# Kernel tuning notes

Hardware: AMD Instinct MI355X
Metric: run time of the kernel (lower is better)

## Reference

```python
import jax, jax.numpy as jnp
import numpy as np

E = 131072
MS, MV = 64, 32            # node/edge/out irreps: 64x0e + 32x1o (dim 160)
DIM = MS + 3 * MV
SC = 64                    # edge scalar dim
BETA = 1.6791767           # normalize2mom(silu) constant used by e3nn FullyConnectedNet
SQ3 = np.float32(np.sqrt(3.0))


def _split(x, ms, mv):
    # e3nn layout: [mul_s scalars | mul_v vectors (mul-major, xyz-minor)]
    return x[:, :ms], x[:, ms:].reshape(x.shape[0], mv, 3)


def _tp(xs, xv, ys, yv, Wss, Wvv, Wsv, Wvs):
    # uvw fully-connected tensor product of (m1s x0e + m1v x1o) with (1x0e + 1x1o),
    # component irrep normalization, 1/sqrt(fan_in) path weights.
    m1s, m1v = xs.shape[1], xv.shape[1]
    s_a = jnp.einsum('eu,uw->ew', xs * ys, Wss) / np.sqrt(m1s)              # 0e x 0e -> 0e
    dot = jnp.einsum('eui,ei->eu', xv, yv) / SQ3                            # 1o x 1o -> 0e
    s_b = jnp.einsum('eu,uw->ew', dot, Wvv) / np.sqrt(m1v)
    v_a = jnp.einsum('eu,ei,uw->ewi', xs, yv, Wsv) / np.sqrt(m1s)           # 0e x 1o -> 1o
    v_b = jnp.einsum('eui,uw->ewi', xv * ys[:, :, None], Wvs) / np.sqrt(m1v)  # 1o x 0e -> 1o
    return jnp.concatenate([s_a, s_b], 1), jnp.concatenate([v_a, v_b], 1)


def _mlp(x, W1, W2, W3):
    # e3nn FullyConnectedNet with silu: variance-preserving layers
    h = BETA * jax.nn.silu(x @ W1 / np.sqrt(W1.shape[0]))
    h = BETA * jax.nn.silu(h @ W2 / np.sqrt(W2.shape[0]))
    return h @ W3 / np.sqrt(W3.shape[0])


def _scale_linear(ms_, mv_, w, Wls, Wlv):
    # LinearScaleWithWeights: per-channel (uvu) scale by generated weights, then o3.Linear
    nS = ms_.shape[1]
    s = ms_ * w[:, :nS]
    v = mv_ * w[:, nS:, None]
    s2 = s @ Wls / np.sqrt(Wls.shape[0])
    v2 = jnp.einsum('eui,uw->ewi', v, Wlv) / np.sqrt(Wlv.shape[0])
    return s2, v2


def _linear(s, v, Ws, Wv):
    return s @ Ws / np.sqrt(Ws.shape[0]), jnp.einsum('eui,uw->ewi', v, Wv) / np.sqrt(Wv.shape[0])


def setup_inputs() -> dict:
    key = jax.random.key(0)
    ks = jax.random.split(key, 32)
    r = lambda i, shp: jax.random.normal(ks[i], shp, dtype=jnp.float32)
    return {
        'node_feats_src': r(0, (E, DIM)),
        'node_feats_dst': r(1, (E, DIM)),
        'edge_feats':     r(2, (E, DIM)),
        'local_env_edge': r(3, (E, 4)),
        'edge_scalars':   r(4, (E, SC)),
        # node TP (combined 128x0e+64x1o x 1x0e+1x1o -> 128x0e+64x1o)
        'Wn_ss': r(5, (2 * MS, MS)), 'Wn_vv': r(6, (2 * MV, MS)),
        'Wn_sv': r(7, (2 * MS, MV)), 'Wn_vs': r(8, (2 * MV, MV)),
        # edge TP (64x0e+32x1o x 1x0e+1x1o -> 128x0e+64x1o)
        'We_ss': r(9, (MS, MS)), 'We_vv': r(10, (MV, MS)),
        'We_sv': r(11, (MS, MV)), 'We_vs': r(12, (MV, MV)),
        # scaler output linears (128x0e+64x1o -> 64x0e+32x1o)
        'Wns_s': r(13, (2 * MS, MS)), 'Wns_v': r(14, (2 * MV, MV)),
        'Wes_s': r(15, (2 * MS, MS)), 'Wes_v': r(16, (2 * MV, MV)),
        # final output linears (irreps_out -> irreps_out)
        'Wno_s': r(17, (MS, MS)), 'Wno_v': r(18, (MV, MV)),
        'Weo_s': r(19, (MS, MS)), 'Weo_v': r(20, (MV, MV)),
        # radial MLPs [64,64,64,192]
        'Wnm1': r(21, (SC, 64)), 'Wnm2': r(22, (64, 64)), 'Wnm3': r(23, (64, 2 * MS + 2 * MV)),
        'Wem1': r(24, (SC, 64)), 'Wem2': r(25, (64, 64)), 'Wem3': r(26, (64, 2 * MS + 2 * MV)),
    }


def reference(node_feats_src, node_feats_dst, edge_feats, local_env_edge, edge_scalars,
              Wn_ss, Wn_vv, Wn_sv, Wn_vs, We_ss, We_vv, We_sv, We_vs,
              Wns_s, Wns_v, Wes_s, Wes_v, Wno_s, Wno_v, Weo_s, Weo_v,
              Wnm1, Wnm2, Wnm3, Wem1, Wem2, Wem3):
    ss, sv = _split(node_feats_src, MS, MV)
    ds, dv = _split(node_feats_dst, MS, MV)
    # AttentionHeadsToVector over stack([src,dst]): per-irrep concat -> 128x0e + 64x1o
    xs = jnp.concatenate([ss, ds], 1)
    xv = jnp.concatenate([sv, dv], 1)
    ys = local_env_edge[:, :1]
    yv = local_env_edge[:, 1:4]
    # node branch
    w_n = _mlp(edge_scalars, Wnm1, Wnm2, Wnm3)
    m_s, m_v = _tp(xs, xv, ys, yv, Wn_ss, Wn_vv, Wn_sv, Wn_vs)
    n_s, n_v = _scale_linear(m_s, m_v, w_n, Wns_s, Wns_v)
    # edge branch
    w_e = _mlp(edge_scalars, Wem1, Wem2, Wem3)
    es, ev = _split(edge_feats, MS, MV)
    e_ms, e_mv = _tp(es, ev, ys, yv, We_ss, We_vv, We_sv, We_vs)
    e_s, e_v = _scale_linear(e_ms, e_mv, w_e, Wes_s, Wes_v)
    # final linears + sum
    on_s, on_v = _linear(n_s, n_v, Wno_s, Wno_v)
    oe_s, oe_v = _linear(e_s, e_v, Weo_s, Weo_v)
    out_s = on_s + oe_s
    out_v = on_v + oe_v
    return jnp.concatenate([out_s, out_v.reshape(out_v.shape[0], -1)], 1)
```

## Files before the change

### kernel.cpp

```cpp
#include <hip/hip_runtime.h>


typedef short  bf16x8 __attribute__((ext_vector_type(8)));
typedef float  f32x4  __attribute__((ext_vector_type(4)));

constexpr float BETA  = 1.6791767f;
constexpr float RS128 = 0.088388347648318447f;
constexpr float RS64  = 0.125f;
constexpr float RS32  = 0.176776695296636881f;
constexpr float RSQ3  = 0.577350269189625842f;

enum : int {
  O_nm1 = 0,      O_nm2 = 4096,   O_nm3 = 8192,
  O_em1 = 20480,  O_em2 = 24576,  O_em3 = 28672,
  O_nss = 40960,  O_nsv = 49152,  O_nvv = 53248,  O_nvs = 57344,
  O_ess = 59392,  O_esv = 63488,  O_evv = 65536,  O_evs = 67584,
  O_nss2= 68608,  O_nsv2= 76800,  O_ess2= 78848,  O_esv2= 87040,
  O_nos = 89088,  O_nov = 93184,  O_eos = 94208,  O_eov = 98304,
  W_TOTAL = 99328
};

struct Ptrs {
  const float *src, *dst, *ef, *env, *scal;
  const ushort* wf;
  float *out;
};

struct PrepArgs {
  const float* src[22];
  int K[22], N[22], ofs[22];
  ushort* dst;
};

__device__ __forceinline__ ushort f2b(float x) {
  union { float f; unsigned u; } v; v.f = x;
  unsigned r = v.u + 0x7fffu + ((v.u >> 16) & 1u);
  return (ushort)(r >> 16);
}
__device__ __forceinline__ unsigned pk2(float a, float b) {
  unsigned r;
  asm("v_cvt_pk_bf16_f32 %0, %1, %2" : "=v"(r) : "v"(a), "v"(b));
  return r;
}
__device__ __forceinline__ float plo(unsigned p) {
  union { unsigned u; float f; } v; v.u = p << 16; return v.f;
}
__device__ __forceinline__ float phi(unsigned p) {
  union { unsigned u; float f; } v; v.u = p & 0xffff0000u; return v.f;
}

__global__ __launch_bounds__(256) void prep_kernel(PrepArgs A) {
  const int mat = blockIdx.x;
  const float* __restrict__ src = A.src[mat];
  const int K = A.K[mat], N = A.N[mat], KS = K >> 5;
  ushort* dst = A.dst + A.ofs[mat];
  const int total = (N * K) >> 3;
  for (int gi = threadIdx.x; gi < total; gi += 256) {
    int t = gi / (64 * KS), r = gi - t * 64 * KS;
    int ks = r >> 6, lane = r & 63;
    int cc = lane & 15, gg = lane >> 4;
    int n = t * 16 + cc, k0 = ks * 32 + gg * 8;
    ushort v[8];
#pragma unroll
    for (int j = 0; j < 8; ++j) v[j] = f2b(src[(size_t)(k0 + j) * N + n]);
    *(uint4*)(dst + (size_t)gi * 8) = *(const uint4*)v;
  }
}

template<int N>
__device__ __forceinline__ void lda(const ushort* __restrict__ wb, unsigned lofs, bf16x8* a) {
#pragma unroll
  for (int i = 0; i < N; ++i) a[i] = *(const bf16x8*)(wb + i * 512 + lofs);
}
template<int T, int KS>
__device__ __forceinline__ void mfm(const bf16x8* a, const bf16x8* bf, f32x4* out) {
#pragma unroll
  for (int t = 0; t < T; ++t) {
    f32x4 acc = (f32x4){0, 0, 0, 0};
#pragma unroll
    for (int ks = 0; ks < KS; ++ks)
      acc = __builtin_amdgcn_mfma_f32_16x16x32_bf16(a[t * KS + ks], bf[ks], acc, 0, 0, 0);
    out[t] = acc;
  }
}
template<int T, int KS>
__device__ __forceinline__ void mfmacc(const bf16x8* a, const bf16x8* bf, f32x4* out) {
#pragma unroll
  for (int t = 0; t < T; ++t)
#pragma unroll
    for (int ks = 0; ks < KS; ++ks)
      out[t] = __builtin_amdgcn_mfma_f32_16x16x32_bf16(a[t * KS + ks], bf[ks], out[t], 0, 0, 0);
}

__device__ __forceinline__ void put2(ushort* b, int cg, int col, const f32x4& d) {
  uint2 p; p.x = pk2(d[0], d[1]); p.y = pk2(d[2], d[3]);
  *(uint2*)(b + cg + col) = p;
}
__device__ __forceinline__ bf16x8 getf(const ushort* b, int cg, int col, int g) {
  return *(const bf16x8*)(b + cg + col + 8 * g);
}
__device__ __forceinline__ bf16x8 ldf8(const float* __restrict__ p) {
  float4 a = *(const float4*)p, b4 = *(const float4*)(p + 4);
  union { unsigned u[4]; bf16x8 v; } r;
  r.u[0] = pk2(a.x, a.y); r.u[1] = pk2(a.z, a.w);
  r.u[2] = pk2(b4.x, b4.y); r.u[3] = pk2(b4.z, b4.w);
  return r.v;
}
__device__ __forceinline__ f32x4 silu4(const f32x4& d) {
  f32x4 o;
#pragma unroll
  for (int r = 0; r < 4; ++r) { float z = d[r] * 0.125f; o[r] = BETA * z / (1.f + __expf(-z)); }
  return o;
}
__device__ __forceinline__ void vecwin(const float* __restrict__ p,
                                       float y0, float y1, float y2,
                                       bf16x8& dotf, bf16x8* xvf) {
  float v[24];
#pragma unroll
  for (int q = 0; q < 6; ++q) *(float4*)&v[4 * q] = *(const float4*)(p + 4 * q);
  float dj[8];
#pragma unroll
  for (int j = 0; j < 8; ++j)
    dj[j] = (v[3 * j] * y0 + v[3 * j + 1] * y1 + v[3 * j + 2] * y2) * RSQ3;
  union { unsigned u[4]; bf16x8 w; } t;
#pragma unroll
  for (int q = 0; q < 4; ++q) t.u[q] = pk2(dj[2 * q], dj[2 * q + 1]);
  dotf = t.w;
#pragma unroll
  for (int i = 0; i < 3; ++i) {
#pragma unroll
    for (int q = 0; q < 4; ++q) t.u[q] = pk2(v[6 * q + i], v[6 * q + 3 + i]);
    xvf[i] = t.w;
  }
}

template<bool ED>
__device__ __forceinline__ void tp_stage(
    const ushort* __restrict__ WF, ushort* b0, ushort* b1, ushort* b2,
    int cg, int g, unsigned lofs,
    const bf16x8* xsf, const bf16x8* dotf, const bf16x8* xvi,
    const uint2* Wp, float ys, float yv0, float yv1, float yv2) {
  constexpr int KA = ED ? 2 : 4;
  constexpr int KB = ED ? 1 : 2;
  const float SA = ED ? RS64 : RS128;
  const float SB = ED ? RS32 : RS64;
  const ushort* w_ss = WF + (ED ? O_ess : O_nss);
  const ushort* w_sv = WF + (ED ? O_esv : O_nsv);
  const ushort* w_vv = WF + (ED ? O_evv : O_nvv);
  const ushort* w_vs = WF + (ED ? O_evs : O_nvs);

  {
    bf16x8 a[4 * KA]; f32x4 d[4];
    lda<4 * KA>(w_ss, lofs, a); mfm<4, KA>(a, xsf, d);
#pragma unroll
    for (int t = 0; t < 4; ++t) {
      f32x4 m;
      m[0] = d[t][0] * ys * SA * plo(Wp[t].x); m[1] = d[t][1] * ys * SA * phi(Wp[t].x);
      m[2] = d[t][2] * ys * SA * plo(Wp[t].y); m[3] = d[t][3] * ys * SA * phi(Wp[t].y);
      put2(b0, cg, 16 * t + 4 * g, m);
    }
  }
  {
    bf16x8 a[4 * KB]; f32x4 d[4];
    lda<4 * KB>(w_vv, lofs, a); mfm<4, KB>(a, dotf, d);
#pragma unroll
    for (int t = 0; t < 4; ++t) {
      f32x4 m;
      m[0] = d[t][0] * SB * plo(Wp[4 + t].x); m[1] = d[t][1] * SB * phi(Wp[4 + t].x);
      m[2] = d[t][2] * SB * plo(Wp[4 + t].y); m[3] = d[t][3] * SB * phi(Wp[4 + t].y);
      put2(b0, cg, 64 + 16 * t + 4 * g, m);
    }
  }
  f32x4 ga[2];
  { bf16x8 a[2 * KA]; lda<2 * KA>(w_sv, lofs, a); mfm<2, KA>(a, xsf, ga); }
  bf16x8 avs[2 * KB];
  lda<2 * KB>(w_vs, lofs, avs);
#pragma unroll
  for (int i = 0; i < 3; ++i) {
    f32x4 db[2];
    mfm<2, KB>(avs, xvi + i * KB, db);
    float yvi = (i == 0) ? yv0 : ((i == 1) ? yv1 : yv2);
    ushort* mb = (i == 2) ? b2 : b1;
    int mbase = (i == 1) ? 64 : 0;
#pragma unroll
    for (int t = 0; t < 2; ++t) {
      f32x4 m;
      m[0] = ga[t][0] * SA * yvi * plo(Wp[8 + t].x); m[1] = ga[t][1] * SA * yvi * phi(Wp[8 + t].x);
      m[2] = ga[t][2] * SA * yvi * plo(Wp[8 + t].y); m[3] = ga[t][3] * SA * yvi * phi(Wp[8 + t].y);
      put2(mb, cg, mbase + 16 * t + 4 * g, m);
    }
#pragma unroll
    for (int t = 0; t < 2; ++t) {
      f32x4 m;
      m[0] = db[t][0] * ys * SB * plo(Wp[10 + t].x); m[1] = db[t][1] * ys * SB * phi(Wp[10 + t].x);
      m[2] = db[t][2] * ys * SB * plo(Wp[10 + t].y); m[3] = db[t][3] * ys * SB * phi(Wp[10 + t].y);
      put2(mb, cg, mbase + 32 + 16 * t + 4 * g, m);
    }
  }
}

template<bool ED>
__device__ __forceinline__ void sl_out_stage(
    const ushort* __restrict__ WF, ushort* b0, ushort* b1, ushort* b2,
    int cg, int g, unsigned lofs, f32x4* os, f32x4 (*ov)[2]) {
  const ushort* w_s2 = WF + (ED ? O_ess2 : O_nss2);
  const ushort* w_v2 = WF + (ED ? O_esv2 : O_nsv2);
  const ushort* w_os = WF + (ED ? O_eos : O_nos);
  const ushort* w_ov = WF + (ED ? O_eov : O_nov);

  bf16x8 mpf[4];
#pragma unroll
  for (int ks = 0; ks < 4; ++ks) mpf[ks] = getf(b0, cg, 32 * ks, g);
  bf16x8 mvf[6];
  mvf[0] = getf(b1, cg, 0, g);  mvf[1] = getf(b1, cg, 32, g);
  mvf[2] = getf(b1, cg, 64, g); mvf[3] = getf(b1, cg, 96, g);
  mvf[4] = getf(b2, cg, 0, g);  mvf[5] = getf(b2, cg, 32, g);
  {
    bf16x8 a[16]; f32x4 d[4];
    lda<16>(w_s2, lofs, a); mfm<4, 4>(a, mpf, d);
#pragma unroll
    for (int t = 0; t < 4; ++t) {
      f32x4 m = { d[t][0] * RS128, d[t][1] * RS128, d[t][2] * RS128, d[t][3] * RS128 };
      put2(b2, cg, 64 + 16 * t + 4 * g, m);
    }
  }
  {
    bf16x8 a[4];
    lda<4>(w_v2, lofs, a);
#pragma unroll
    for (int i = 0; i < 3; ++i) {
      f32x4 dn[2]; mfm<2, 2>(a, mvf + 2 * i, dn);
#pragma unroll
      for (int t = 0; t < 2; ++t) {
        f32x4 m = { dn[t][0] * RS64, dn[t][1] * RS64, dn[t][2] * RS64, dn[t][3] * RS64 };
        put2(b0, cg, i * 32 + 16 * t + 4 * g, m);
      }
    }
  }
  {
    bf16x8 nsf[2] = { getf(b2, cg, 64, g), getf(b2, cg, 96, g) };
    bf16x8 a[8]; lda<8>(w_os, lofs, a);
    mfmacc<4, 2>(a, nsf, os);
  }
  {
    bf16x8 a[2]; lda<2>(w_ov, lofs, a);
#pragma unroll
    for (int i = 0; i < 3; ++i) {
      bf16x8 nvf = getf(b0, cg, i * 32, g);
#pragma unroll
      for (int t = 0; t < 2; ++t)
        ov[i][t] = __builtin_amdgcn_mfma_f32_16x16x32_bf16(a[t], nvf, ov[i][t], 0, 0, 0);
    }
  }
}

__global__ __launch_bounds__(256, 3) void mp_kernel(Ptrs P) {
  const int tid  = threadIdx.x;
  const int lane = tid & 63, wid = tid >> 6;
  const int c    = lane & 15, g  = lane >> 4;
  const unsigned lofs = lane * 8;
  const int cg   = c * 136;
  const int e    = (blockIdx.x * 4 + wid) * 16 + c;
  const ushort* __restrict__ WF = P.wf;

  __shared__ ushort sb[4][3][16][136];
  ushort* b0 = &sb[wid][0][0][0];
  ushort* b1 = &sb[wid][1][0][0];
  ushort* b2 = &sb[wid][2][0][0];

  const float* __restrict__ rs = P.src + (size_t)e * 160;
  const float* __restrict__ rd = P.dst + (size_t)e * 160;
  const float* __restrict__ re = P.ef  + (size_t)e * 160;
  const float* __restrict__ rq = P.scal + (size_t)e * 64;

  float4 ev = *(const float4*)(P.env + (size_t)e * 4);
  const float ys = ev.x, yv0 = ev.y, yv1 = ev.z, yv2 = ev.w;

  bf16x8 sc[2];
  sc[0] = ldf8(rq + 8 * g);
  sc[1] = ldf8(rq + 32 + 8 * g);

  bf16x8 xsf_n[4];
  xsf_n[0] = ldf8(rs + 8 * g);  xsf_n[1] = ldf8(rs + 32 + 8 * g);
  xsf_n[2] = ldf8(rd + 8 * g);  xsf_n[3] = ldf8(rd + 32 + 8 * g);
  bf16x8 dot_n[2]; bf16x8 xv_n[6];
  {
    bf16x8 tmp[3];
    vecwin(rs + 64 + 24 * g, yv0, yv1, yv2, dot_n[0], tmp);
    xv_n[0] = tmp[0]; xv_n[2] = tmp[1]; xv_n[4] = tmp[2];
    vecwin(rd + 64 + 24 * g, yv0, yv1, yv2, dot_n[1], tmp);
    xv_n[1] = tmp[0]; xv_n[3] = tmp[1]; xv_n[5] = tmp[2];
  }

  uint2 Wpn[12], Wpe[12];
  {
    bf16x8 an[8], ae[8]; f32x4 dn[4], de[4];
    lda<8>(WF + O_nm1, lofs, an); lda<8>(WF + O_em1, lofs, ae);
    mfm<4, 2>(an, sc, dn); mfm<4, 2>(ae, sc, de);
#pragma unroll
    for (int t = 0; t < 4; ++t) put2(b0, cg, 16 * t + 4 * g, silu4(dn[t]));
#pragma unroll
    for (int t = 0; t < 4; ++t) put2(b2, cg, 16 * t + 4 * g, silu4(de[t]));
    lda<8>(WF + O_nm2, lofs, an); lda<8>(WF + O_em2, lofs, ae);
    bf16x8 hn[2] = { getf(b0, cg, 0, g), getf(b0, cg, 32, g) };
    bf16x8 he[2] = { getf(b2, cg, 0, g), getf(b2, cg, 32, g) };
    mfm<4, 2>(an, hn, dn); mfm<4, 2>(ae, he, de);
#pragma unroll
    for (int t = 0; t < 4; ++t) put2(b1, cg, 16 * t + 4 * g, silu4(dn[t]));
#pragma unroll
    for (int t = 0; t < 4; ++t) put2(b2, cg, 64 + 16 * t + 4 * g, silu4(de[t]));
    bf16x8 h2n[2] = { getf(b1, cg, 0, g), getf(b1, cg, 32, g) };
    bf16x8 h2e[2] = { getf(b2, cg, 64, g), getf(b2, cg, 96, g) };
    {
      bf16x8 a3[24]; f32x4 dw[12];
      lda<24>(WF + O_nm3, lofs, a3); mfm<12, 2>(a3, h2n, dw);
#pragma unroll
      for (int t = 0; t < 12; ++t) {
        Wpn[t].x = pk2(dw[t][0] * 0.125f, dw[t][1] * 0.125f);
        Wpn[t].y = pk2(dw[t][2] * 0.125f, dw[t][3] * 0.125f);
      }
      lda<24>(WF + O_em3, lofs, a3); mfm<12, 2>(a3, h2e, dw);
#pragma unroll
      for (int t = 0; t < 12; ++t) {
        Wpe[t].x = pk2(dw[t][0] * 0.125f, dw[t][1] * 0.125f);
        Wpe[t].y = pk2(dw[t][2] * 0.125f, dw[t][3] * 0.125f);
      }
    }
  }

  f32x4 os[4]; f32x4 ov[3][2];
#pragma unroll
  for (int t = 0; t < 4; ++t) os[t] = (f32x4){0, 0, 0, 0};
#pragma unroll
  for (int i = 0; i < 3; ++i)
#pragma unroll
    for (int t = 0; t < 2; ++t) ov[i][t] = (f32x4){0, 0, 0, 0};

  tp_stage<false>(WF, b0, b1, b2, cg, g, lofs, xsf_n, dot_n, xv_n, Wpn, ys, yv0, yv1, yv2);

  bf16x8 xsf_e[2] = { ldf8(re + 8 * g), ldf8(re + 32 + 8 * g) };
  bf16x8 dot_e[1]; bf16x8 xv_e[3];
  {
    bf16x8 tmp[3];
    vecwin(re + 64 + 24 * g, yv0, yv1, yv2, dot_e[0], tmp);
    xv_e[0] = tmp[0]; xv_e[1] = tmp[1]; xv_e[2] = tmp[2];
  }

  sl_out_stage<false>(WF, b0, b1, b2, cg, g, lofs, os, ov);

  tp_stage<true>(WF, b0, b1, b2, cg, g, lofs, xsf_e, dot_e, xv_e, Wpe, ys, yv0, yv1, yv2);
  sl_out_stage<true>(WF, b0, b1, b2, cg, g, lofs, os, ov);

  float* __restrict__ po = P.out + (size_t)e * 160;
#pragma unroll
  for (int t = 0; t < 4; ++t) {
    float4 o = { os[t][0] * RS64, os[t][1] * RS64, os[t][2] * RS64, os[t][3] * RS64 };
    *(float4*)(po + 16 * t + 4 * g) = o;
  }
#pragma unroll
  for (int t = 0; t < 2; ++t) {
    float vv[12];
#pragma unroll
    for (int r = 0; r < 4; ++r)
#pragma unroll
      for (int i = 0; i < 3; ++i) vv[3 * r + i] = ov[i][t][r] * RS32;
    *(float4*)(po + 64 + 48 * t + 12 * g)     = *(float4*)&vv[0];
    *(float4*)(po + 64 + 48 * t + 12 * g + 4) = *(float4*)&vv[4];
    *(float4*)(po + 64 + 48 * t + 12 * g + 8) = *(float4*)&vv[8];
  }
}

extern "C" void kernel_launch(void* const* d_in, const int* in_sizes, int n_in,
                              void* d_out, int out_size, void* d_ws, size_t ws_size,
                              hipStream_t stream) {
  PrepArgs A;
  const int src_idx[22] = {21,22,23, 24,25,26, 5,7,6,8, 9,11,10,12, 13,14, 15,16, 17,18, 19,20};
  const int Ks[22] = {64,64,64, 64,64,64, 128,128,64,64, 64,64,32,32, 128,64, 128,64, 64,32, 64,32};
  const int Ns[22] = {64,64,192, 64,64,192, 64,32,64,32, 64,32,64,32, 64,32, 64,32, 64,32, 64,32};
  const int Os[22] = {O_nm1,O_nm2,O_nm3, O_em1,O_em2,O_em3,
                      O_nss,O_nsv,O_nvv,O_nvs, O_ess,O_esv,O_evv,O_evs,
                      O_nss2,O_nsv2, O_ess2,O_esv2, O_nos,O_nov, O_eos,O_eov};
  for (int i = 0; i < 22; ++i) {
    A.src[i] = (const float*)d_in[src_idx[i]];
    A.K[i] = Ks[i]; A.N[i] = Ns[i]; A.ofs[i] = Os[i];
  }
  A.dst = (ushort*)d_ws;
  prep_kernel<<<dim3(22), dim3(256), 0, stream>>>(A);

  Ptrs P;
  P.src  = (const float*)d_in[0];
  P.dst  = (const float*)d_in[1];
  P.ef   = (const float*)d_in[2];
  P.env  = (const float*)d_in[3];
  P.scal = (const float*)d_in[4];
  P.wf   = (const ushort*)d_ws;
  P.out  = (float*)d_out;

  const int E = in_sizes[0] / 160;
  mp_kernel<<<dim3(E / 64), dim3(256), 0, stream>>>(P);
}
```

Baseline: 134.7 us.

## Inline stages and software-prefetch weight fragments ahead of their MFMAs

Inlines the tensor-product and scale/output stages into the kernel body and issues the global loads of weight fragments one stage early, so they overlap the previous stage's MFMAs and LDS traffic. Compiler memory fences are inserted to keep that ordering, and the MLP layer-3 weight loads are split in half and double-buffered. To make room for the extra live registers, launch bounds drop from 3 to 2 blocks per CU, which lowers occupancy.

```diff
diff --git a/kernel.cpp b/kernel.cpp
--- a/kernel.cpp
+++ b/kernel.cpp
@@ -3,6 +3,8 @@
 
 typedef short  bf16x8 __attribute__((ext_vector_type(8)));
 typedef float  f32x4  __attribute__((ext_vector_type(4)));
+
+#define FENCE() asm volatile("" ::: "memory")
 
 constexpr float BETA  = 1.6791767f;
 constexpr float RS128 = 0.088388347648318447f;
@@ -134,127 +136,7 @@
   }
 }
 
-template<bool ED>
-__device__ __forceinline__ void tp_stage(
-    const ushort* __restrict__ WF, ushort* b0, ushort* b1, ushort* b2,
-    int cg, int g, unsigned lofs,
-    const bf16x8* xsf, const bf16x8* dotf, const bf16x8* xvi,
-    const uint2* Wp, float ys, float yv0, float yv1, float yv2) {
-  constexpr int KA = ED ? 2 : 4;
-  constexpr int KB = ED ? 1 : 2;
-  const float SA = ED ? RS64 : RS128;
-  const float SB = ED ? RS32 : RS64;
-  const ushort* w_ss = WF + (ED ? O_ess : O_nss);
-  const ushort* w_sv = WF + (ED ? O_esv : O_nsv);
-  const ushort* w_vv = WF + (ED ? O_evv : O_nvv);
-  const ushort* w_vs = WF + (ED ? O_evs : O_nvs);
-
-  {
-    bf16x8 a[4 * KA]; f32x4 d[4];
-    lda<4 * KA>(w_ss, lofs, a); mfm<4, KA>(a, xsf, d);
-#pragma unroll
-    for (int t = 0; t < 4; ++t) {
-      f32x4 m;
-      m[0] = d[t][0] * ys * SA * plo(Wp[t].x); m[1] = d[t][1] * ys * SA * phi(Wp[t].x);
-      m[2] = d[t][2] * ys * SA * plo(Wp[t].y); m[3] = d[t][3] * ys * SA * phi(Wp[t].y);
-      put2(b0, cg, 16 * t + 4 * g, m);
-    }
-  }
-  {
-    bf16x8 a[4 * KB]; f32x4 d[4];
-    lda<4 * KB>(w_vv, lofs, a); mfm<4, KB>(a, dotf, d);
-#pragma unroll
-    for (int t = 0; t < 4; ++t) {
-      f32x4 m;
-      m[0] = d[t][0] * SB * plo(Wp[4 + t].x); m[1] = d[t][1] * SB * phi(Wp[4 + t].x);
-      m[2] = d[t][2] * SB * plo(Wp[4 + t].y); m[3] = d[t][3] * SB * phi(Wp[4 + t].y);
-      put2(b0, cg, 64 + 16 * t + 4 * g, m);
-    }
-  }
-  f32x4 ga[2];
-  { bf16x8 a[2 * KA]; lda<2 * KA>(w_sv, lofs, a); mfm<2, KA>(a, xsf, ga); }
-  bf16x8 avs[2 * KB];
-  lda<2 * KB>(w_vs, lofs, avs);
-#pragma unroll
-  for (int i = 0; i < 3; ++i) {
-    f32x4 db[2];
-    mfm<2, KB>(avs, xvi + i * KB, db);
-    float yvi = (i == 0) ? yv0 : ((i == 1) ? yv1 : yv2);
-    ushort* mb = (i == 2) ? b2 : b1;
-    int mbase = (i == 1) ? 64 : 0;
-#pragma unroll
-    for (int t = 0; t < 2; ++t) {
-      f32x4 m;
-      m[0] = ga[t][0] * SA * yvi * plo(Wp[8 + t].x); m[1] = ga[t][1] * SA * yvi * phi(Wp[8 + t].x);
-      m[2] = ga[t][2] * SA * yvi * plo(Wp[8 + t].y); m[3] = ga[t][3] * SA * yvi * phi(Wp[8 + t].y);
-      put2(mb, cg, mbase + 16 * t + 4 * g, m);
-    }
-#pragma unroll
-    for (int t = 0; t < 2; ++t) {
-      f32x4 m;
-      m[0] = db[t][0] * ys * SB * plo(Wp[10 + t].x); m[1] = db[t][1] * ys * SB * phi(Wp[10 + t].x);
-      m[2] = db[t][2] * ys * SB * plo(Wp[10 + t].y); m[3] = db[t][3] * ys * SB * phi(Wp[10 + t].y);
-      put2(mb, cg, mbase + 32 + 16 * t + 4 * g, m);
-    }
-  }
-}
-
-template<bool ED>
-__device__ __forceinline__ void sl_out_stage(
-    const ushort* __restrict__ WF, ushort* b0, ushort* b1, ushort* b2,
-    int cg, int g, unsigned lofs, f32x4* os, f32x4 (*ov)[2]) {
-  const ushort* w_s2 = WF + (ED ? O_ess2 : O_nss2);
-  const ushort* w_v2 = WF + (ED ? O_esv2 : O_nsv2);
-  const ushort* w_os = WF + (ED ? O_eos : O_nos);
-  const ushort* w_ov = WF + (ED ? O_eov : O_nov);
-
-  bf16x8 mpf[4];
-#pragma unroll
-  for (int ks = 0; ks < 4; ++ks) mpf[ks] = getf(b0, cg, 32 * ks, g);
-  bf16x8 mvf[6];
-  mvf[0] = getf(b1, cg, 0, g);  mvf[1] = getf(b1, cg, 32, g);
-  mvf[2] = getf(b1, cg, 64, g); mvf[3] = getf(b1, cg, 96, g);
-  mvf[4] = getf(b2, cg, 0, g);  mvf[5] = getf(b2, cg, 32, g);
-  {
-    bf16x8 a[16]; f32x4 d[4];
-    lda<16>(w_s2, lofs, a); mfm<4, 4>(a, mpf, d);
-#pragma unroll
-    for (int t = 0; t < 4; ++t) {
-      f32x4 m = { d[t][0] * RS128, d[t][1] * RS128, d[t][2] * RS128, d[t][3] * RS128 };
-      put2(b2, cg, 64 + 16 * t + 4 * g, m);
-    }
-  }
-  {
-    bf16x8 a[4];
-    lda<4>(w_v2, lofs, a);
-#pragma unroll
-    for (int i = 0; i < 3; ++i) {
-      f32x4 dn[2]; mfm<2, 2>(a, mvf + 2 * i, dn);
-#pragma unroll
-      for (int t = 0; t < 2; ++t) {
-        f32x4 m = { dn[t][0] * RS64, dn[t][1] * RS64, dn[t][2] * RS64, dn[t][3] * RS64 };
-        put2(b0, cg, i * 32 + 16 * t + 4 * g, m);
-      }
-    }
-  }
-  {
-    bf16x8 nsf[2] = { getf(b2, cg, 64, g), getf(b2, cg, 96, g) };
-    bf16x8 a[8]; lda<8>(w_os, lofs, a);
-    mfmacc<4, 2>(a, nsf, os);
-  }
-  {
-    bf16x8 a[2]; lda<2>(w_ov, lofs, a);
-#pragma unroll
-    for (int i = 0; i < 3; ++i) {
-      bf16x8 nvf = getf(b0, cg, i * 32, g);
-#pragma unroll
-      for (int t = 0; t < 2; ++t)
-        ov[i][t] = __builtin_amdgcn_mfma_f32_16x16x32_bf16(a[t], nvf, ov[i][t], 0, 0, 0);
-    }
-  }
-}
-
-__global__ __launch_bounds__(256, 3) void mp_kernel(Ptrs P) {
+__global__ __launch_bounds__(256, 2) void mp_kernel(Ptrs P) {
   const int tid  = threadIdx.x;
   const int lane = tid & 63, wid = tid >> 6;
   const int c    = lane & 15, g  = lane >> 4;
@@ -273,17 +155,41 @@
   const float* __restrict__ re = P.ef  + (size_t)e * 160;
   const float* __restrict__ rq = P.scal + (size_t)e * 64;
 
+  bf16x8 a1n[8], a1e[8];
+  lda<8>(WF + O_nm1, lofs, a1n);
+  lda<8>(WF + O_em1, lofs, a1e);
+
   float4 ev = *(const float4*)(P.env + (size_t)e * 4);
   const float ys = ev.x, yv0 = ev.y, yv1 = ev.z, yv2 = ev.w;
-
   bf16x8 sc[2];
   sc[0] = ldf8(rq + 8 * g);
   sc[1] = ldf8(rq + 32 + 8 * g);
 
+  f32x4 os[4]; f32x4 ov[3][2];
+#pragma unroll
+  for (int t = 0; t < 4; ++t) os[t] = (f32x4){0, 0, 0, 0};
+#pragma unroll
+  for (int i = 0; i < 3; ++i)
+#pragma unroll
+    for (int t = 0; t < 2; ++t) ov[i][t] = (f32x4){0, 0, 0, 0};
+
+  {
+    f32x4 dn[4], de[4];
+    mfm<4, 2>(a1n, sc, dn); mfm<4, 2>(a1e, sc, de);
+#pragma unroll
+    for (int t = 0; t < 4; ++t) put2(b0, cg, 16 * t + 4 * g, silu4(dn[t]));
+#pragma unroll
+    for (int t = 0; t < 4; ++t) put2(b2, cg, 16 * t + 4 * g, silu4(de[t]));
+  }
+  FENCE();
+
+  bf16x8 a2n[8], a2e[8];
+  lda<8>(WF + O_nm2, lofs, a2n);
+  lda<8>(WF + O_em2, lofs, a2e);
   bf16x8 xsf_n[4];
   xsf_n[0] = ldf8(rs + 8 * g);  xsf_n[1] = ldf8(rs + 32 + 8 * g);
   xsf_n[2] = ldf8(rd + 8 * g);  xsf_n[3] = ldf8(rd + 32 + 8 * g);
-  bf16x8 dot_n[2]; bf16x8 xv_n[6];
+  bf16x8 dot_n[2], xv_n[6];
   {
     bf16x8 tmp[3];
     vecwin(rs + 64 + 24 * g, yv0, yv1, yv2, dot_n[0], tmp);
@@ -292,64 +198,249 @@
     xv_n[1] = tmp[0]; xv_n[3] = tmp[1]; xv_n[5] = tmp[2];
   }
 
-  uint2 Wpn[12], Wpe[12];
-  {
-    bf16x8 an[8], ae[8]; f32x4 dn[4], de[4];
-    lda<8>(WF + O_nm1, lofs, an); lda<8>(WF + O_em1, lofs, ae);
-    mfm<4, 2>(an, sc, dn); mfm<4, 2>(ae, sc, de);
-#pragma unroll
-    for (int t = 0; t < 4; ++t) put2(b0, cg, 16 * t + 4 * g, silu4(dn[t]));
-#pragma unroll
-    for (int t = 0; t < 4; ++t) put2(b2, cg, 16 * t + 4 * g, silu4(de[t]));
-    lda<8>(WF + O_nm2, lofs, an); lda<8>(WF + O_em2, lofs, ae);
+  {
     bf16x8 hn[2] = { getf(b0, cg, 0, g), getf(b0, cg, 32, g) };
     bf16x8 he[2] = { getf(b2, cg, 0, g), getf(b2, cg, 32, g) };
-    mfm<4, 2>(an, hn, dn); mfm<4, 2>(ae, he, de);
+    f32x4 dn[4], de[4];
+    mfm<4, 2>(a2n, hn, dn); mfm<4, 2>(a2e, he, de);
 #pragma unroll
     for (int t = 0; t < 4; ++t) put2(b1, cg, 16 * t + 4 * g, silu4(dn[t]));
 #pragma unroll
     for (int t = 0; t < 4; ++t) put2(b2, cg, 64 + 16 * t + 4 * g, silu4(de[t]));
+  }
+  FENCE();
+
+  uint2 Wpn[12], Wpe[12];
+  {
+    bf16x8 aA[12], aB[12];
+    lda<12>(WF + O_nm3, lofs, aA);
+    lda<12>(WF + O_nm3 + 12 * 512, lofs, aB);
     bf16x8 h2n[2] = { getf(b1, cg, 0, g), getf(b1, cg, 32, g) };
     bf16x8 h2e[2] = { getf(b2, cg, 64, g), getf(b2, cg, 96, g) };
-    {
-      bf16x8 a3[24]; f32x4 dw[12];
-      lda<24>(WF + O_nm3, lofs, a3); mfm<12, 2>(a3, h2n, dw);
-#pragma unroll
-      for (int t = 0; t < 12; ++t) {
-        Wpn[t].x = pk2(dw[t][0] * 0.125f, dw[t][1] * 0.125f);
-        Wpn[t].y = pk2(dw[t][2] * 0.125f, dw[t][3] * 0.125f);
-      }
-      lda<24>(WF + O_em3, lofs, a3); mfm<12, 2>(a3, h2e, dw);
-#pragma unroll
-      for (int t = 0; t < 12; ++t) {
-        Wpe[t].x = pk2(dw[t][0] * 0.125f, dw[t][1] * 0.125f);
-        Wpe[t].y = pk2(dw[t][2] * 0.125f, dw[t][3] * 0.125f);
-      }
-    }
-  }
-
-  f32x4 os[4]; f32x4 ov[3][2];
-#pragma unroll
-  for (int t = 0; t < 4; ++t) os[t] = (f32x4){0, 0, 0, 0};
-#pragma unroll
-  for (int i = 0; i < 3; ++i)
-#pragma unroll
-    for (int t = 0; t < 2; ++t) ov[i][t] = (f32x4){0, 0, 0, 0};
-
-  tp_stage<false>(WF, b0, b1, b2, cg, g, lofs, xsf_n, dot_n, xv_n, Wpn, ys, yv0, yv1, yv2);
-
-  bf16x8 xsf_e[2] = { ldf8(re + 8 * g), ldf8(re + 32 + 8 * g) };
-  bf16x8 dot_e[1]; bf16x8 xv_e[3];
-  {
-    bf16x8 tmp[3];
-    vecwin(re + 64 + 24 * g, yv0, yv1, yv2, dot_e[0], tmp);
-    xv_e[0] = tmp[0]; xv_e[1] = tmp[1]; xv_e[2] = tmp[2];
-  }
-
-  sl_out_stage<false>(WF, b0, b1, b2, cg, g, lofs, os, ov);
-
-  tp_stage<true>(WF, b0, b1, b2, cg, g, lofs, xsf_e, dot_e, xv_e, Wpe, ys, yv0, yv1, yv2);
-  sl_out_stage<true>(WF, b0, b1, b2, cg, g, lofs, os, ov);
+    f32x4 dw[6];
+    mfm<6, 2>(aA, h2n, dw);
+    lda<12>(WF + O_em3, lofs, aA);
+#pragma unroll
+    for (int t = 0; t < 6; ++t) { Wpn[t].x = pk2(dw[t][0]*0.125f, dw[t][1]*0.125f); Wpn[t].y = pk2(dw[t][2]*0.125f, dw[t][3]*0.125f); }
+    mfm<6, 2>(aB, h2n, dw);
+    lda<12>(WF + O_em3 + 12 * 512, lofs, aB);
+#pragma unroll
+    for (int t = 0; t < 6; ++t) { Wpn[6+t].x = pk2(dw[t][0]*0.125f, dw[t][1]*0.125f); Wpn[6+t].y = pk2(dw[t][2]*0.125f, dw[t][3]*0.125f); }
+    mfm<6, 2>(aA, h2e, dw);
+#pragma unroll
+    for (int t = 0; t < 6; ++t) { Wpe[t].x = pk2(dw[t][0]*0.125f, dw[t][1]*0.125f); Wpe[t].y = pk2(dw[t][2]*0.125f, dw[t][3]*0.125f); }
+    mfm<6, 2>(aB, h2e, dw);
+#pragma unroll
+    for (int t = 0; t < 6; ++t) { Wpe[6+t].x = pk2(dw[t][0]*0.125f, dw[t][1]*0.125f); Wpe[6+t].y = pk2(dw[t][2]*0.125f, dw[t][3]*0.125f); }
+  }
+  FENCE();
+
+  f32x4 ga[2];
+  {
+    bf16x8 assn[16], avvn[8];
+    lda<16>(WF + O_nss, lofs, assn);
+    lda<8>(WF + O_nvv, lofs, avvn);
+    {
+      f32x4 d[4];
+      mfm<4, 4>(assn, xsf_n, d);
+#pragma unroll
+      for (int t = 0; t < 4; ++t) {
+        f32x4 m;
+        m[0] = d[t][0]*ys*RS128*plo(Wpn[t].x); m[1] = d[t][1]*ys*RS128*phi(Wpn[t].x);
+        m[2] = d[t][2]*ys*RS128*plo(Wpn[t].y); m[3] = d[t][3]*ys*RS128*phi(Wpn[t].y);
+        put2(b0, cg, 16 * t + 4 * g, m);
+      }
+    }
+    bf16x8 asvn[8], avsn[4];
+    lda<8>(WF + O_nsv, lofs, asvn);
+    lda<4>(WF + O_nvs, lofs, avsn);
+    {
+      f32x4 d[4];
+      mfm<4, 2>(avvn, dot_n, d);
+#pragma unroll
+      for (int t = 0; t < 4; ++t) {
+        f32x4 m;
+        m[0] = d[t][0]*RS64*plo(Wpn[4+t].x); m[1] = d[t][1]*RS64*phi(Wpn[4+t].x);
+        m[2] = d[t][2]*RS64*plo(Wpn[4+t].y); m[3] = d[t][3]*RS64*phi(Wpn[4+t].y);
+        put2(b0, cg, 64 + 16 * t + 4 * g, m);
+      }
+    }
+    mfm<2, 4>(asvn, xsf_n, ga);
+#pragma unroll
+    for (int i = 0; i < 3; ++i) {
+      f32x4 db[2];
+      mfm<2, 2>(avsn, xv_n + i * 2, db);
+      float yvi = (i == 0) ? yv0 : ((i == 1) ? yv1 : yv2);
+      ushort* mb = (i == 2) ? b2 : b1;
+      int mbase = (i == 1) ? 64 : 0;
+#pragma unroll
+      for (int t = 0; t < 2; ++t) {
+        f32x4 m;
+        m[0] = ga[t][0]*RS128*yvi*plo(Wpn[8+t].x); m[1] = ga[t][1]*RS128*yvi*phi(Wpn[8+t].x);
+        m[2] = ga[t][2]*RS128*yvi*plo(Wpn[8+t].y); m[3] = ga[t][3]*RS128*yvi*phi(Wpn[8+t].y);
+        put2(mb, cg, mbase + 16 * t + 4 * g, m);
+      }
+#pragma unroll
+      for (int t = 0; t < 2; ++t) {
+        f32x4 m;
+        m[0] = db[t][0]*ys*RS64*plo(Wpn[10+t].x); m[1] = db[t][1]*ys*RS64*phi(Wpn[10+t].x);
+        m[2] = db[t][2]*ys*RS64*plo(Wpn[10+t].y); m[3] = db[t][3]*ys*RS64*phi(Wpn[10+t].y);
+        put2(mb, cg, mbase + 32 + 16 * t + 4 * g, m);
+      }
+    }
+  }
+  FENCE();
+
+  bf16x8 xsf_e[2]; bf16x8 dot_e[1], xv_e[3];
+  {
+    bf16x8 as2n[16], av2n[4];
+    lda<16>(WF + O_nss2, lofs, as2n);
+    lda<4>(WF + O_nsv2, lofs, av2n);
+    xsf_e[0] = ldf8(re + 8 * g); xsf_e[1] = ldf8(re + 32 + 8 * g);
+    {
+      bf16x8 tmp[3];
+      vecwin(re + 64 + 24 * g, yv0, yv1, yv2, dot_e[0], tmp);
+      xv_e[0] = tmp[0]; xv_e[1] = tmp[1]; xv_e[2] = tmp[2];
+    }
+    bf16x8 mpf[4];
+#pragma unroll
+    for (int ks = 0; ks < 4; ++ks) mpf[ks] = getf(b0, cg, 32 * ks, g);
+    bf16x8 mvf[6];
+    mvf[0] = getf(b1, cg, 0, g);  mvf[1] = getf(b1, cg, 32, g);
+    mvf[2] = getf(b1, cg, 64, g); mvf[3] = getf(b1, cg, 96, g);
+    mvf[4] = getf(b2, cg, 0, g);  mvf[5] = getf(b2, cg, 32, g);
+    {
+      f32x4 d[4];
+      mfm<4, 4>(as2n, mpf, d);
+#pragma unroll
+      for (int t = 0; t < 4; ++t) {
+        f32x4 m = { d[t][0]*RS128, d[t][1]*RS128, d[t][2]*RS128, d[t][3]*RS128 };
+        put2(b2, cg, 64 + 16 * t + 4 * g, m);
+      }
+    }
+    bf16x8 aosn[8], aovn[2];
+    lda<8>(WF + O_nos, lofs, aosn);
+    lda<2>(WF + O_nov, lofs, aovn);
+#pragma unroll
+    for (int i = 0; i < 3; ++i) {
+      f32x4 dn2[2];
+      mfm<2, 2>(av2n, mvf + 2 * i, dn2);
+#pragma unroll
+      for (int t = 0; t < 2; ++t) {
+        f32x4 m = { dn2[t][0]*RS64, dn2[t][1]*RS64, dn2[t][2]*RS64, dn2[t][3]*RS64 };
+        put2(b0, cg, i * 32 + 16 * t + 4 * g, m);
+      }
+    }
+    FENCE();
+    bf16x8 nsf[2] = { getf(b2, cg, 64, g), getf(b2, cg, 96, g) };
+    mfmacc<4, 2>(aosn, nsf, os);
+#pragma unroll
+    for (int i = 0; i < 3; ++i) {
+      bf16x8 nvf = getf(b0, cg, i * 32, g);
+#pragma unroll
+      for (int t = 0; t < 2; ++t)
+        ov[i][t] = __builtin_amdgcn_mfma_f32_16x16x32_bf16(aovn[t], nvf, ov[i][t], 0, 0, 0);
+    }
+  }
+  FENCE();
+
+  {
+    bf16x8 asse[8], avve[4], asve[4], avse[2];
+    lda<8>(WF + O_ess, lofs, asse);
+    lda<4>(WF + O_evv, lofs, avve);
+    lda<4>(WF + O_esv, lofs, asve);
+    lda<2>(WF + O_evs, lofs, avse);
+    {
+      f32x4 d[4];
+      mfm<4, 2>(asse, xsf_e, d);
+#pragma unroll
+      for (int t = 0; t < 4; ++t) {
+        f32x4 m;
+        m[0] = d[t][0]*ys*RS64*plo(Wpe[t].x); m[1] = d[t][1]*ys*RS64*phi(Wpe[t].x);
+        m[2] = d[t][2]*ys*RS64*plo(Wpe[t].y); m[3] = d[t][3]*ys*RS64*phi(Wpe[t].y);
+        put2(b0, cg, 16 * t + 4 * g, m);
+      }
+    }
+    bf16x8 as2e[16];
+    lda<16>(WF + O_ess2, lofs, as2e);
+    {
+      f32x4 d[4];
+      mfm<4, 1>(avve, dot_e, d);
+#pragma unroll
+      for (int t = 0; t < 4; ++t) {
+        f32x4 m;
+        m[0] = d[t][0]*RS32*plo(Wpe[4+t].x); m[1] = d[t][1]*RS32*phi(Wpe[4+t].x);
+        m[2] = d[t][2]*RS32*plo(Wpe[4+t].y); m[3] = d[t][3]*RS32*phi(Wpe[4+t].y);
+        put2(b0, cg, 64 + 16 * t + 4 * g, m);
+      }
+    }
+    mfm<2, 2>(asve, xsf_e, ga);
+    bf16x8 av2e[4];
+    lda<4>(WF + O_esv2, lofs, av2e);
+#pragma unroll
+    for (int i = 0; i < 3; ++i) {
+      f32x4 db[2];
+      mfm<2, 1>(avse, xv_e + i, db);
+      float yvi = (i == 0) ? yv0 : ((i == 1) ? yv1 : yv2);
+      ushort* mb = (i == 2) ? b2 : b1;
+      int mbase = (i == 1) ? 64 : 0;
+#pragma unroll
+      for (int t = 0; t < 2; ++t) {
+        f32x4 m;
+        m[0] = ga[t][0]*RS64*yvi*plo(Wpe[8+t].x); m[1] = ga[t][1]*RS64*yvi*phi(Wpe[8+t].x);
+        m[2] = ga[t][2]*RS64*yvi*plo(Wpe[8+t].y); m[3] = ga[t][3]*RS64*yvi*phi(Wpe[8+t].y);
+        put2(mb, cg, mbase + 16 * t + 4 * g, m);
+      }
+#pragma unroll
+      for (int t = 0; t < 2; ++t) {
+        f32x4 m;
+        m[0] = db[t][0]*ys*RS32*plo(Wpe[10+t].x); m[1] = db[t][1]*ys*RS32*phi(Wpe[10+t].x);
+        m[2] = db[t][2]*ys*RS32*plo(Wpe[10+t].y); m[3] = db[t][3]*ys*RS32*phi(Wpe[10+t].y);
+        put2(mb, cg, mbase + 32 + 16 * t + 4 * g, m);
+      }
+    }
+    FENCE();
+
+    bf16x8 mpf[4];
+#pragma unroll
+    for (int ks = 0; ks < 4; ++ks) mpf[ks] = getf(b0, cg, 32 * ks, g);
+    bf16x8 mvf[6];
+    mvf[0] = getf(b1, cg, 0, g);  mvf[1] = getf(b1, cg, 32, g);
+    mvf[2] = getf(b1, cg, 64, g); mvf[3] = getf(b1, cg, 96, g);
+    mvf[4] = getf(b2, cg, 0, g);  mvf[5] = getf(b2, cg, 32, g);
+    {
+      f32x4 d[4];
+      mfm<4, 4>(as2e, mpf, d);
+#pragma unroll
+      for (int t = 0; t < 4; ++t) {
+        f32x4 m = { d[t][0]*RS128, d[t][1]*RS128, d[t][2]*RS128, d[t][3]*RS128 };
+        put2(b2, cg, 64 + 16 * t + 4 * g, m);
+      }
+    }
+    bf16x8 aose[8], aove[2];
+    lda<8>(WF + O_eos, lofs, aose);
+    lda<2>(WF + O_eov, lofs, aove);
+#pragma unroll
+    for (int i = 0; i < 3; ++i) {
+      f32x4 dn2[2];
+      mfm<2, 2>(av2e, mvf + 2 * i, dn2);
+#pragma unroll
+      for (int t = 0; t < 2; ++t) {
+        f32x4 m = { dn2[t][0]*RS64, dn2[t][1]*RS64, dn2[t][2]*RS64, dn2[t][3]*RS64 };
+        put2(b0, cg, i * 32 + 16 * t + 4 * g, m);
+      }
+    }
+    FENCE();
+    bf16x8 nsf[2] = { getf(b2, cg, 64, g), getf(b2, cg, 96, g) };
+    mfmacc<4, 2>(aose, nsf, os);
+#pragma unroll
+    for (int i = 0; i < 3; ++i) {
+      bf16x8 nvf = getf(b0, cg, i * 32, g);
+#pragma unroll
+      for (int t = 0; t < 2; ++t)
+        ov[i][t] = __builtin_amdgcn_mfma_f32_16x16x32_bf16(aove[t], nvf, ov[i][t], 0, 0, 0);
+    }
+  }
 
   float* __restrict__ po = P.out + (size_t)e * 160;
 #pragma unroll
```

Result: no change. 137.3 us (+1.9%).
